# Kernel optimization log

Measured on AMD Instinct MI355X. Metric: run time of the kernel, lower is better.

## Reference

```python
import jax, jax.numpy as jnp
import numpy as np

N_EMB = 100000
DIM = 64
BATCH = 16384
HIST = 200


def setup_inputs() -> dict:
    key = jax.random.key(0)
    k_idx, k_w = jax.random.split(key)
    indices = jax.random.randint(k_idx, (BATCH, HIST), 0, N_EMB, dtype=jnp.int64 if jax.config.jax_enable_x64 else jnp.int32)
    # torch.nn.Linear(n_embeddings, dim, bias=False) weight has shape [dim, n_embeddings]
    W = jax.random.normal(k_w, (DIM, N_EMB), dtype=jnp.float32)
    return {"indices": indices, "W": W}


def reference(indices, W):
    # Original: onehot(indices) [B,H,N] @ W.T [N,D]  ==  gather of W.T rows.
    # Same math expressed as a direct lookup (no N x N eye materialized).
    table = W.T  # [n_embeddings, dim]
    return table[indices]  # [BATCH, HIST, dim]
```

## Files before the change

### kernel.cpp

```cpp
#include <hip/hip_runtime.h>

#define N_EMB 100000
#define DIM   64

typedef float    f32x4 __attribute__((ext_vector_type(4)));
typedef _Float16 f16x4 __attribute__((ext_vector_type(4)));

__global__ void transpose_w_h(const float* __restrict__ W,
                              _Float16* __restrict__ table,
                              int n_emb) {
    __shared__ float tile[64][65];
    const int n0   = blockIdx.x * 64;
    const int t    = threadIdx.x;
    const int lane = t & 63;
    const int grp  = t >> 6;

    #pragma unroll
    for (int i = 0; i < 16; ++i) {
        const int d = grp * 16 + i;
        const int n = n0 + lane;
        tile[d][lane] = (n < n_emb) ? W[(long long)d * N_EMB + n] : 0.0f;
    }
    __syncthreads();

    #pragma unroll
    for (int i = 0; i < 16; ++i) {
        const int n = n0 + grp * 16 + i;
        if (n < n_emb)
            table[(long long)n * DIM + lane] = (_Float16)tile[lane][grp * 16 + i];
    }
}

__device__ __forceinline__ void store_stream(f32x4* p, f32x4 v) {
    asm volatile("global_store_dwordx4 %0, %1, off sc0 sc1 nt"
                 :: "v"(p), "v"(v) : "memory");
}

__global__ void __launch_bounds__(256) gather_h4(
        const int* __restrict__ idx,
        const f16x4* __restrict__ tableh,
        f32x4* __restrict__ out4,
        long long total_f4) {
    const long long stride = (long long)gridDim.x * blockDim.x;
    for (long long g = (long long)blockIdx.x * blockDim.x + threadIdx.x;
         g < total_f4; g += stride) {
        const int id = idx[g >> 4];
        const f16x4 h = tableh[(long long)id * 16 + (int)(g & 15)];
        const f32x4 v = __builtin_convertvector(h, f32x4);
        store_stream(out4 + g, v);
    }
}

__global__ void gather_direct(const int* __restrict__ idx,
                              const float* __restrict__ W,
                              float* __restrict__ out,
                              long long total) {
    const long long stride = (long long)gridDim.x * blockDim.x;
    for (long long g = (long long)blockIdx.x * blockDim.x + threadIdx.x;
         g < total; g += stride) {
        out[g] = W[(long long)(g & 63) * N_EMB + idx[g >> 6]];
    }
}

extern "C" void kernel_launch(void* const* d_in, const int* in_sizes, int n_in,
                              void* d_out, int out_size, void* d_ws, size_t ws_size,
                              hipStream_t stream) {
    const int*   idx = (const int*)d_in[0];
    const float* W   = (const float*)d_in[1];
    float*       out = (float*)d_out;

    const long long total     = (long long)out_size;
    const size_t    tbl_bytes = (size_t)N_EMB * DIM * sizeof(_Float16);

    if (ws_size >= tbl_bytes) {
        _Float16* table = (_Float16*)d_ws;

        transpose_w_h<<<(N_EMB + 63) / 64, 256, 0, stream>>>(W, table, N_EMB);

        const long long total_f4 = total / 4;
        gather_h4<<<2048, 256, 0, stream>>>(idx, (const f16x4*)table,
                                            (f32x4*)out, total_f4);
    } else {
        gather_direct<<<2048, 256, 0, stream>>>(idx, W, out, total);
    }
}
```

Before: 180.7 us.

## Split fp16 table into dimension slices and gather in four passes

```diff
diff --git a/kernel.cpp b/kernel.cpp
--- a/kernel.cpp
+++ b/kernel.cpp
@@ -3,12 +3,15 @@
 #define N_EMB 100000
 #define DIM   64
 
+#define NPASS  4
+#define DSLICE (DIM / NPASS)
+
 typedef float    f32x4 __attribute__((ext_vector_type(4)));
 typedef _Float16 f16x4 __attribute__((ext_vector_type(4)));
 
-__global__ void transpose_w_h(const float* __restrict__ W,
-                              _Float16* __restrict__ table,
-                              int n_emb) {
+__global__ void transpose_w_sliced(const float* __restrict__ W,
+                                   _Float16* __restrict__ tbl,
+                                   int n_emb) {
     __shared__ float tile[64][65];
     const int n0   = blockIdx.x * 64;
     const int t    = threadIdx.x;
@@ -26,8 +29,12 @@
     #pragma unroll
     for (int i = 0; i < 16; ++i) {
         const int n = n0 + grp * 16 + i;
-        if (n < n_emb)
-            table[(long long)n * DIM + lane] = (_Float16)tile[lane][grp * 16 + i];
+        if (n < n_emb) {
+            const int d = lane;
+            const long long a =
+                ((long long)(d >> 4) * n_emb + n) * DSLICE + (d & 15);
+            tbl[a] = (_Float16)tile[lane][grp * 16 + i];
+        }
     }
 }
 
@@ -36,18 +43,20 @@
                  :: "v"(p), "v"(v) : "memory");
 }
 
-__global__ void __launch_bounds__(256) gather_h4(
+__global__ void __launch_bounds__(256) gather_pass(
         const int* __restrict__ idx,
-        const f16x4* __restrict__ tableh,
-        f32x4* __restrict__ out4,
-        long long total_f4) {
+        const f16x4* __restrict__ slice,
+        f32x4* __restrict__ outp,
+        long long nq) {
     const long long stride = (long long)gridDim.x * blockDim.x;
-    for (long long g = (long long)blockIdx.x * blockDim.x + threadIdx.x;
-         g < total_f4; g += stride) {
-        const int id = idx[g >> 4];
-        const f16x4 h = tableh[(long long)id * 16 + (int)(g & 15)];
+    for (long long q = (long long)blockIdx.x * blockDim.x + threadIdx.x;
+         q < nq; q += stride) {
+        const long long row = q >> 2;
+        const int       e   = (int)(q & 3);
+        const int       id  = idx[row];
+        const f16x4 h = slice[(long long)id * 4 + e];
         const f32x4 v = __builtin_convertvector(h, f32x4);
-        store_stream(out4 + g, v);
+        store_stream(outp + row * 16 + e, v);
     }
 }
 
@@ -69,17 +78,21 @@
     const float* W   = (const float*)d_in[1];
     float*       out = (float*)d_out;
 
+    const long long n_idx     = (long long)in_sizes[0];
     const long long total     = (long long)out_size;
     const size_t    tbl_bytes = (size_t)N_EMB * DIM * sizeof(_Float16);
 
     if (ws_size >= tbl_bytes) {
-        _Float16* table = (_Float16*)d_ws;
+        _Float16* tbl = (_Float16*)d_ws;
 
-        transpose_w_h<<<(N_EMB + 63) / 64, 256, 0, stream>>>(W, table, N_EMB);
+        transpose_w_sliced<<<(N_EMB + 63) / 64, 256, 0, stream>>>(W, tbl, N_EMB);
 
-        const long long total_f4 = total / 4;
-        gather_h4<<<2048, 256, 0, stream>>>(idx, (const f16x4*)table,
-                                            (f32x4*)out, total_f4);
+        const long long nq = n_idx * 4;
+        for (int p = 0; p < NPASS; ++p) {
+            const f16x4* slice = (const f16x4*)tbl + (long long)p * N_EMB * 4;
+            f32x4*       outp  = (f32x4*)out + p * 4;
+            gather_pass<<<2048, 256, 0, stream>>>(idx, slice, outp, nq);
+        }
     } else {
         gather_direct<<<2048, 256, 0, stream>>>(idx, W, out, total);
     }
```

After: 238.7 us. 1.32x slower.
